# Performance work log

Measured on AMD Instinct MI355X. Metric: run time of the kernel, lower is better.

The kernel has to match this reference:

```python
import jax, jax.numpy as jnp
import numpy as np

N, IN_DIM, OUT_DIM, H = 8192, 512, 512, 1
BN_EPS = 1e-5


def _lin(key, fan_in, fan_out):
    k1, k2 = jax.random.split(key)
    b = 1.0 / np.sqrt(fan_in)
    W = jax.random.uniform(k1, (fan_in, fan_out), jnp.float32, -b, b)
    bias = jax.random.uniform(k2, (fan_out,), jnp.float32, -b, b)
    return W, bias


def setup_inputs() -> dict:
    key = jax.random.key(0)
    ks = jax.random.split(key, 12)
    h = jax.random.normal(ks[0], (N, IN_DIM), jnp.float32)
    A = (jax.random.uniform(ks[1], (N, N)) < 0.01).astype(jnp.float32)
    qw, qb = _lin(ks[2], IN_DIM, OUT_DIM * H)
    kw, kb = _lin(ks[3], IN_DIM, OUT_DIM * H)
    vw, vb = _lin(ks[4], IN_DIM, OUT_DIM * H)
    ow, ob = _lin(ks[5], OUT_DIM, OUT_DIM)
    f1w, f1b = _lin(ks[6], OUT_DIM, OUT_DIM * 2)
    f2w, f2b = _lin(ks[7], OUT_DIM * 2, OUT_DIM)
    bn1_g = jax.random.normal(ks[8], (OUT_DIM,)) * 0.1 + 1.0
    bn1_b = jax.random.normal(ks[9], (OUT_DIM,)) * 0.1
    bn1_m = jax.random.normal(ks[10], (OUT_DIM,)) * 0.1
    bn1_v = jax.random.uniform(ks[11], (OUT_DIM,), jnp.float32, 0.5, 1.5)
    ks2 = jax.random.split(jax.random.fold_in(key, 7), 4)
    bn2_g = jax.random.normal(ks2[0], (OUT_DIM,)) * 0.1 + 1.0
    bn2_b = jax.random.normal(ks2[1], (OUT_DIM,)) * 0.1
    bn2_m = jax.random.normal(ks2[2], (OUT_DIM,)) * 0.1
    bn2_v = jax.random.uniform(ks2[3], (OUT_DIM,), jnp.float32, 0.5, 1.5)
    return dict(A=A, h=h, qw=qw, qb=qb, kw=kw, kb=kb, vw=vw, vb=vb,
                ow=ow, ob=ob, f1w=f1w, f1b=f1b, f2w=f2w, f2b=f2b,
                bn1_g=bn1_g, bn1_b=bn1_b, bn1_m=bn1_m, bn1_v=bn1_v,
                bn2_g=bn2_g, bn2_b=bn2_b, bn2_m=bn2_m, bn2_v=bn2_v)


def _bn_eval(x, g, b, m, v):
    return (x - m) * jax.lax.rsqrt(v + BN_EPS) * g + b


def reference(A, h, qw, qb, kw, kb, vw, vb, ow, ob, f1w, f1b, f2w, f2b,
              bn1_g, bn1_b, bn1_m, bn1_v, bn2_g, bn2_b, bn2_m, bn2_v):
    n = h.shape[0]
    scaling = OUT_DIM ** (-0.5)
    # q/k/v: [N, D, H] as in torch reshape of [N, D*H]
    q = (h @ qw + qb).reshape(n, OUT_DIM, H) * scaling
    k = (h @ kw + kb).reshape(n, OUT_DIM, H)
    v = (h @ vw + vb).reshape(n, OUT_DIM, H)
    qh = jnp.transpose(q, (2, 0, 1))          # (H, N, D)
    kh = jnp.transpose(k, (2, 1, 0))          # (H, D, N)
    vh = jnp.transpose(v, (2, 0, 1))          # (H, N, D)
    attn = jnp.einsum('hnd,hdm->hnm', qh, kh) * A[None]   # (H, N, N)
    attn = jax.nn.softmax(attn, axis=0)        # NOTE: softmax over HEAD axis, as in source
    out = jnp.einsum('hnm,hmd->hnd', attn, vh).reshape(n, H * OUT_DIM)
    # GTLayer (eval mode: dropout = identity, BN uses running stats)
    x = out @ ow + ob
    x = x + h                                  # residual
    x = _bn_eval(x, bn1_g, bn1_b, bn1_m, bn1_v)
    h2 = x
    f = jax.nn.relu(x @ f1w + f1b) @ f2w + f2b
    x = h2 + f
    x = _bn_eval(x, bn2_g, bn2_b, bn2_m, bn2_v)
    return x
```

## Files before the change

### kernel.cpp

```cpp
#include <hip/hip_runtime.h>

#define NROWS 8192
#define DIM 512
#define HID 1024
#define BN_EPS 1e-5f

typedef unsigned short ushort_t;
typedef __attribute__((ext_vector_type(8))) __bf16 bf16x8;
typedef __attribute__((ext_vector_type(4))) float f32x4;

union U4 {
    uint4 u;
    bf16x8 b;
    ushort_t s[8];
};

static __device__ __forceinline__ float b2f(ushort_t u) {
    union { float f; unsigned int i; } c;
    c.i = ((unsigned int)u) << 16;
    return c.f;
}

static __device__ __forceinline__ ushort_t f2b(float f) {
    union { float f; unsigned int i; } c;
    c.f = f;
    unsigned int i = c.i;
    unsigned int r = (i + 0x7FFFu + ((i >> 16) & 1u)) >> 16;
    return (ushort_t)r;
}

__global__ void colsum_convert_kernel(const float* __restrict__ h, float* __restrict__ hs,
                                      ushort_t* __restrict__ hB) {
    int t = threadIdx.x;
    int col0 = (t & 127) * 4;
    int rsub = t >> 7;
    int row0 = blockIdx.x * 32;
    float acc[4] = {0.f, 0.f, 0.f, 0.f};
    for (int r = 0; r < 16; ++r) {
        int row = row0 + r * 2 + rsub;
        float4 v = *(const float4*)(h + (size_t)row * DIM + col0);
        acc[0] += v.x; acc[1] += v.y; acc[2] += v.z; acc[3] += v.w;
        ushort_t bv[4];
        bv[0] = f2b(v.x); bv[1] = f2b(v.y); bv[2] = f2b(v.z); bv[3] = f2b(v.w);
        *(uint2*)(hB + (size_t)row * DIM + col0) = *(uint2*)bv;
    }
#pragma unroll
    for (int j = 0; j < 4; ++j) atomicAdd(&hs[col0 + j], acc[j]);
}

__global__ void matvec_kernel(const float* __restrict__ xin, const float* __restrict__ W,
                              const float* __restrict__ bvec, float scaleB,
                              float* __restrict__ outv, int ncols) {
    __shared__ float red[8][32];
    int t = threadIdx.x;
    int col = blockIdx.x * 32 + (t & 31);
    int ks = t >> 5;
    float s = 0.f;
    for (int ki = 0; ki < 64; ++ki) {
        int k = ks * 64 + ki;
        s += xin[k] * W[(size_t)k * ncols + col];
    }
    red[ks][t & 31] = s;
    __syncthreads();
    if (ks == 0) {
        float tot = scaleB * bvec[col];
#pragma unroll
        for (int r = 0; r < 8; ++r) tot += red[r][t & 31];
        outv[col] = tot;
    }
}

__global__ void matvec_b1p_kernel(const float* __restrict__ tvec,
                                  const float* __restrict__ g1, const float* __restrict__ b1,
                                  const float* __restrict__ m1, const float* __restrict__ v1,
                                  const float* __restrict__ W, const float* __restrict__ bvec,
                                  float* __restrict__ outv) {
    __shared__ float red[8][32];
    int t = threadIdx.x;
    int col = blockIdx.x * 32 + (t & 31);
    int ks = t >> 5;
    float s = 0.f;
    for (int ki = 0; ki < 64; ++ki) {
        int k = ks * 64 + ki;
        float a1 = g1[k] * rsqrtf(v1[k] + BN_EPS);
        float q0 = tvec[k] * a1 + (b1[k] - m1[k] * a1);
        s += q0 * W[(size_t)k * HID + col];
    }
    red[ks][t & 31] = s;
    __syncthreads();
    if (ks == 0) {
        float tot = bvec[col];
#pragma unroll
        for (int r = 0; r < 8; ++r) tot += red[r][t & 31];
        outv[col] = tot;
    }
}

__global__ void prepw_kernel(const float* __restrict__ f1w,
                             const float* __restrict__ g1, const float* __restrict__ v1,
                             const float* __restrict__ f2w,
                             ushort_t* __restrict__ W1T, ushort_t* __restrict__ W2T) {
    __shared__ float tile[32][33];
    int tx = threadIdx.x & 31, ty = threadIdx.x >> 5;
    int b = blockIdx.x;
    if (b < 512) {
        int bx = (b & 31) * 32, by = (b >> 5) * 32;
#pragma unroll
        for (int i = 0; i < 32; i += 8)
            tile[ty + i][tx] = f1w[(size_t)(by + ty + i) * HID + bx + tx];
        __syncthreads();
        int r = by + tx;
        float a1 = g1[r] * rsqrtf(v1[r] + BN_EPS);
#pragma unroll
        for (int i = 0; i < 32; i += 8)
            W1T[(size_t)(bx + ty + i) * DIM + r] = f2b(tile[tx][ty + i] * a1);
    } else {
        int b2 = b - 512;
        int bx = (b2 & 15) * 32, by = (b2 >> 4) * 32;
#pragma unroll
        for (int i = 0; i < 32; i += 8)
            tile[ty + i][tx] = f2w[(size_t)(by + ty + i) * DIM + bx + tx];
        __syncthreads();
#pragma unroll
        for (int i = 0; i < 32; i += 8)
            W2T[(size_t)(bx + ty + i) * HID + by + tx] = f2b(tile[tx][ty + i]);
    }
}

__global__ __launch_bounds__(256) void gemm1_kernel(const ushort_t* __restrict__ A,
                                                    const ushort_t* __restrict__ BT,
                                                    const float* __restrict__ bias,
                                                    ushort_t* __restrict__ C) {
    const int K = DIM, Nn = HID, BK = 32, LDA = BK + 8;
    __shared__ ushort_t As[128 * LDA];
    __shared__ ushort_t Bs[128 * LDA];
    int tid = threadIdx.x;
    int lane = tid & 63, w = tid >> 6;
    int wm = (w & 1) * 64, wn = (w >> 1) * 64;
    int bm = blockIdx.y * 128, bn = blockIdx.x * 128;

    f32x4 acc[4][4] = {};

    int r0 = tid >> 2, kc0 = (tid & 3) * 8;
    int r1 = r0 + 64;

    for (int k0 = 0; k0 < K; k0 += BK) {
        __syncthreads();
        uint4 a0 = *(const uint4*)(A + (size_t)(bm + r0) * K + k0 + kc0);
        uint4 a1 = *(const uint4*)(A + (size_t)(bm + r1) * K + k0 + kc0);
        uint4 b0 = *(const uint4*)(BT + (size_t)(bn + r0) * K + k0 + kc0);
        uint4 b1 = *(const uint4*)(BT + (size_t)(bn + r1) * K + k0 + kc0);
        *(uint4*)(As + r0 * LDA + kc0) = a0;
        *(uint4*)(As + r1 * LDA + kc0) = a1;
        *(uint4*)(Bs + r0 * LDA + kc0) = b0;
        *(uint4*)(Bs + r1 * LDA + kc0) = b1;
        __syncthreads();

        int koff = (lane >> 4) * 8;
        bf16x8 af[4], bfr[4];
#pragma unroll
        for (int i = 0; i < 4; ++i) {
            U4 t;
            t.u = *(const uint4*)(As + (wm + i * 16 + (lane & 15)) * LDA + koff);
            af[i] = t.b;
        }
#pragma unroll
        for (int j = 0; j < 4; ++j) {
            U4 t;
            t.u = *(const uint4*)(Bs + (wn + j * 16 + (lane & 15)) * LDA + koff);
            bfr[j] = t.b;
        }
#pragma unroll
        for (int i = 0; i < 4; ++i)
#pragma unroll
            for (int j = 0; j < 4; ++j)
                acc[i][j] = __builtin_amdgcn_mfma_f32_16x16x32_bf16(af[i], bfr[j], acc[i][j], 0, 0, 0);
    }

#pragma unroll
    for (int i = 0; i < 4; ++i) {
        int row0 = bm + wm + i * 16 + (lane >> 4) * 4;
#pragma unroll
        for (int j = 0; j < 4; ++j) {
            int col = bn + wn + j * 16 + (lane & 15);
            float bv = bias[col];
#pragma unroll
            for (int r = 0; r < 4; ++r) {
                float v = fmaxf(acc[i][j][r] + bv, 0.f);
                C[(size_t)(row0 + r) * Nn + col] = f2b(v);
            }
        }
    }
}

__global__ __launch_bounds__(256) void gemm2_kernel(const ushort_t* __restrict__ A,
                                                    const ushort_t* __restrict__ BT,
                                                    const float* __restrict__ bias,
                                                    const ushort_t* __restrict__ hB,
                                                    const float* __restrict__ tvec,
                                                    const float* __restrict__ g1,
                                                    const float* __restrict__ b1,
                                                    const float* __restrict__ m1,
                                                    const float* __restrict__ v1,
                                                    const float* __restrict__ g2,
                                                    const float* __restrict__ b2,
                                                    const float* __restrict__ m2,
                                                    const float* __restrict__ v2,
                                                    float* __restrict__ out) {
    const int K = HID, BK = 32, LDA = BK + 8;
    __shared__ ushort_t As[128 * LDA];
    __shared__ ushort_t Bs[64 * LDA];
    int tid = threadIdx.x;
    int lane = tid & 63, w = tid >> 6;
    int wm = (w & 1) * 64, wn = (w >> 1) * 32;
    int bm = blockIdx.y * 128, bn = blockIdx.x * 64;

    f32x4 acc[4][2] = {};

    int r0 = tid >> 2, kc0 = (tid & 3) * 8;
    int r1 = r0 + 64;

    for (int k0 = 0; k0 < K; k0 += BK) {
        __syncthreads();
        uint4 a0 = *(const uint4*)(A + (size_t)(bm + r0) * K + k0 + kc0);
        uint4 a1 = *(const uint4*)(A + (size_t)(bm + r1) * K + k0 + kc0);
        uint4 bb = *(const uint4*)(BT + (size_t)(bn + r0) * K + k0 + kc0);
        *(uint4*)(As + r0 * LDA + kc0) = a0;
        *(uint4*)(As + r1 * LDA + kc0) = a1;
        *(uint4*)(Bs + r0 * LDA + kc0) = bb;
        __syncthreads();

        int koff = (lane >> 4) * 8;
        bf16x8 af[4], bfr[2];
#pragma unroll
        for (int i = 0; i < 4; ++i) {
            U4 t;
            t.u = *(const uint4*)(As + (wm + i * 16 + (lane & 15)) * LDA + koff);
            af[i] = t.b;
        }
#pragma unroll
        for (int j = 0; j < 2; ++j) {
            U4 t;
            t.u = *(const uint4*)(Bs + (wn + j * 16 + (lane & 15)) * LDA + koff);
            bfr[j] = t.b;
        }
#pragma unroll
        for (int i = 0; i < 4; ++i)
#pragma unroll
            for (int j = 0; j < 2; ++j)
                acc[i][j] = __builtin_amdgcn_mfma_f32_16x16x32_bf16(af[i], bfr[j], acc[i][j], 0, 0, 0);
    }

#pragma unroll
    for (int i = 0; i < 4; ++i) {
        int row0 = bm + wm + i * 16 + (lane >> 4) * 4;
#pragma unroll
        for (int j = 0; j < 2; ++j) {
            int col = bn + wn + j * 16 + (lane & 15);
            float a1c = g1[col] * rsqrtf(v1[col] + BN_EPS);
            float q0c = tvec[col] * a1c + (b1[col] - m1[col] * a1c);
            float a2c = g2[col] * rsqrtf(v2[col] + BN_EPS);
            float c2c = b2[col] - m2[col] * a2c;
            float bv = bias[col];
#pragma unroll
            for (int r = 0; r < 4; ++r) {
                int row = row0 + r;
                float x1 = b2f(hB[(size_t)row * DIM + col]) * a1c + q0c;
                out[(size_t)row * DIM + col] = (x1 + acc[i][j][r] + bv) * a2c + c2c;
            }
        }
    }
}

extern "C" void kernel_launch(void* const* d_in, const int* in_sizes, int n_in,
                              void* d_out, int out_size, void* d_ws, size_t ws_size,
                              hipStream_t stream) {
    const float* h = (const float*)d_in[1];
    const float* vw = (const float*)d_in[6];
    const float* vb = (const float*)d_in[7];
    const float* ow = (const float*)d_in[8];
    const float* ob = (const float*)d_in[9];
    const float* f1w = (const float*)d_in[10];
    const float* f1b = (const float*)d_in[11];
    const float* f2w = (const float*)d_in[12];
    const float* fb2 = (const float*)d_in[13];
    const float* g1 = (const float*)d_in[14];
    const float* b1 = (const float*)d_in[15];
    const float* m1 = (const float*)d_in[16];
    const float* v1 = (const float*)d_in[17];
    const float* g2 = (const float*)d_in[18];
    const float* b2 = (const float*)d_in[19];
    const float* m2 = (const float*)d_in[20];
    const float* v2 = (const float*)d_in[21];
    float* out = (float*)d_out;

    char* ws = (char*)d_ws;
    float* hs = (float*)(ws + 0);
    float* sBuf = (float*)(ws + 4096);
    float* tBuf = (float*)(ws + 8192);
    float* b1P = (float*)(ws + 16384);
    ushort_t* W1T = (ushort_t*)(ws + 32768);
    ushort_t* W2T = (ushort_t*)(ws + 32768 + 1048576);
    ushort_t* Z = (ushort_t*)(ws + 32768 + 2097152);
    ushort_t* hB = (ushort_t*)(ws + 32768 + 2097152 + 16777216);

    hipMemsetAsync(hs, 0, 512 * sizeof(float), stream);
    colsum_convert_kernel<<<256, 256, 0, stream>>>(h, hs, hB);
    matvec_kernel<<<16, 256, 0, stream>>>(hs, vw, vb, 8192.0f, sBuf, 512);
    matvec_kernel<<<16, 256, 0, stream>>>(sBuf, ow, ob, 1.0f, tBuf, 512);
    matvec_b1p_kernel<<<32, 256, 0, stream>>>(tBuf, g1, b1, m1, v1, f1w, f1b, b1P);
    prepw_kernel<<<1024, 256, 0, stream>>>(f1w, g1, v1, f2w, W1T, W2T);
    gemm1_kernel<<<dim3(8, 64), 256, 0, stream>>>(hB, W1T, b1P, Z);
    gemm2_kernel<<<dim3(8, 64), 256, 0, stream>>>(Z, W2T, fb2, hB, tBuf,
                                                  g1, b1, m1, v1, g2, b2, m2, v2, out);
}
```

Measured before the change: 471.1 us.

## Use direct global-to-LDS loads with XOR swizzle, BK=64, and fuse matvecs

Both GEMMs now stage tiles with global_load_lds (direct global-to-LDS DMA) over a 64-wide K tile and an XOR-swizzled LDS layout. This removes the register round trip and the padded layout and halves the number of barriers per K. The three small matvec kernels become one single-block kernel that also precomputes the per-column BN coefficients, so the gemm2 epilogue no longer recomputes rsqrt. The trade-off is that the fused matvec runs in one block of 512 threads, serializing work that was previously spread over 16 to 32 blocks.

```diff
diff --git a/kernel.cpp b/kernel.cpp
--- a/kernel.cpp
+++ b/kernel.cpp
@@ -8,6 +8,11 @@
 typedef unsigned short ushort_t;
 typedef __attribute__((ext_vector_type(8))) __bf16 bf16x8;
 typedef __attribute__((ext_vector_type(4))) float f32x4;
+
+typedef __attribute__((address_space(3))) void lds_void_t;
+typedef const __attribute__((address_space(1))) void gbl_void_t;
+
+#define GLDS16(g, l) __builtin_amdgcn_global_load_lds((gbl_void_t*)(g), (lds_void_t*)(l), 16, 0, 0)
 
 union U4 {
     uint4 u;
@@ -48,51 +53,40 @@
     for (int j = 0; j < 4; ++j) atomicAdd(&hs[col0 + j], acc[j]);
 }
 
-__global__ void matvec_kernel(const float* __restrict__ xin, const float* __restrict__ W,
-                              const float* __restrict__ bvec, float scaleB,
-                              float* __restrict__ outv, int ncols) {
-    __shared__ float red[8][32];
+__global__ void small_fused_kernel(const float* __restrict__ hs,
+                                   const float* __restrict__ vw, const float* __restrict__ vb,
+                                   const float* __restrict__ ow, const float* __restrict__ ob,
+                                   const float* __restrict__ f1w, const float* __restrict__ f1b,
+                                   const float* __restrict__ g1, const float* __restrict__ b1,
+                                   const float* __restrict__ m1, const float* __restrict__ v1,
+                                   const float* __restrict__ g2, const float* __restrict__ b2,
+                                   const float* __restrict__ m2, const float* __restrict__ v2,
+                                   float* __restrict__ cA1, float* __restrict__ cQ0,
+                                   float* __restrict__ cA2, float* __restrict__ cC2,
+                                   float* __restrict__ b1P) {
+    __shared__ float sh[512];
     int t = threadIdx.x;
-    int col = blockIdx.x * 32 + (t & 31);
-    int ks = t >> 5;
-    float s = 0.f;
-    for (int ki = 0; ki < 64; ++ki) {
-        int k = ks * 64 + ki;
-        s += xin[k] * W[(size_t)k * ncols + col];
-    }
-    red[ks][t & 31] = s;
+    float acc = 8192.0f * vb[t];
+    for (int k = 0; k < 512; ++k) acc += hs[k] * vw[(size_t)k * 512 + t];
+    sh[t] = acc;
     __syncthreads();
-    if (ks == 0) {
-        float tot = scaleB * bvec[col];
-#pragma unroll
-        for (int r = 0; r < 8; ++r) tot += red[r][t & 31];
-        outv[col] = tot;
-    }
-}
-
-__global__ void matvec_b1p_kernel(const float* __restrict__ tvec,
-                                  const float* __restrict__ g1, const float* __restrict__ b1,
-                                  const float* __restrict__ m1, const float* __restrict__ v1,
-                                  const float* __restrict__ W, const float* __restrict__ bvec,
-                                  float* __restrict__ outv) {
-    __shared__ float red[8][32];
-    int t = threadIdx.x;
-    int col = blockIdx.x * 32 + (t & 31);
-    int ks = t >> 5;
-    float s = 0.f;
-    for (int ki = 0; ki < 64; ++ki) {
-        int k = ks * 64 + ki;
-        float a1 = g1[k] * rsqrtf(v1[k] + BN_EPS);
-        float q0 = tvec[k] * a1 + (b1[k] - m1[k] * a1);
-        s += q0 * W[(size_t)k * HID + col];
-    }
-    red[ks][t & 31] = s;
+    float acc2 = ob[t];
+    for (int k = 0; k < 512; ++k) acc2 += sh[k] * ow[(size_t)k * 512 + t];
+    float a1 = g1[t] * rsqrtf(v1[t] + BN_EPS);
+    float q0 = acc2 * a1 + (b1[t] - m1[t] * a1);
+    float a2 = g2[t] * rsqrtf(v2[t] + BN_EPS);
+    cA1[t] = a1;
+    cQ0[t] = q0;
+    cA2[t] = a2;
+    cC2[t] = b2[t] - m2[t] * a2;
     __syncthreads();
-    if (ks == 0) {
-        float tot = bvec[col];
-#pragma unroll
-        for (int r = 0; r < 8; ++r) tot += red[r][t & 31];
-        outv[col] = tot;
+    sh[t] = q0;
+    __syncthreads();
+#pragma unroll
+    for (int c = t; c < 1024; c += 512) {
+        float a = f1b[c];
+        for (int k = 0; k < 512; ++k) a += sh[k] * f1w[(size_t)k * HID + c];
+        b1P[c] = a;
     }
 }
 
@@ -131,9 +125,9 @@
                                                     const ushort_t* __restrict__ BT,
                                                     const float* __restrict__ bias,
                                                     ushort_t* __restrict__ C) {
-    const int K = DIM, Nn = HID, BK = 32, LDA = BK + 8;
-    __shared__ ushort_t As[128 * LDA];
-    __shared__ ushort_t Bs[128 * LDA];
+    const int K = DIM, Nn = HID;
+    __shared__ ushort_t As[128 * 64];
+    __shared__ ushort_t Bs[128 * 64];
     int tid = threadIdx.x;
     int lane = tid & 63, w = tid >> 6;
     int wm = (w & 1) * 64, wn = (w >> 1) * 64;
@@ -141,40 +135,48 @@
 
     f32x4 acc[4][4] = {};
 
-    int r0 = tid >> 2, kc0 = (tid & 3) * 8;
-    int r1 = r0 + 64;
-
-    for (int k0 = 0; k0 < K; k0 += BK) {
-        __syncthreads();
-        uint4 a0 = *(const uint4*)(A + (size_t)(bm + r0) * K + k0 + kc0);
-        uint4 a1 = *(const uint4*)(A + (size_t)(bm + r1) * K + k0 + kc0);
-        uint4 b0 = *(const uint4*)(BT + (size_t)(bn + r0) * K + k0 + kc0);
-        uint4 b1 = *(const uint4*)(BT + (size_t)(bn + r1) * K + k0 + kc0);
-        *(uint4*)(As + r0 * LDA + kc0) = a0;
-        *(uint4*)(As + r1 * LDA + kc0) = a1;
-        *(uint4*)(Bs + r0 * LDA + kc0) = b0;
-        *(uint4*)(Bs + r1 * LDA + kc0) = b1;
-        __syncthreads();
-
-        int koff = (lane >> 4) * 8;
-        bf16x8 af[4], bfr[4];
-#pragma unroll
-        for (int i = 0; i < 4; ++i) {
-            U4 t;
-            t.u = *(const uint4*)(As + (wm + i * 16 + (lane & 15)) * LDA + koff);
-            af[i] = t.b;
-        }
-#pragma unroll
-        for (int j = 0; j < 4; ++j) {
-            U4 t;
-            t.u = *(const uint4*)(Bs + (wn + j * 16 + (lane & 15)) * LDA + koff);
-            bfr[j] = t.b;
-        }
-#pragma unroll
-        for (int i = 0; i < 4; ++i)
-#pragma unroll
-            for (int j = 0; j < 4; ++j)
-                acc[i][j] = __builtin_amdgcn_mfma_f32_16x16x32_bf16(af[i], bfr[j], acc[i][j], 0, 0, 0);
+    int rsub = tid >> 3;
+    int clog = (tid & 7) ^ (rsub & 7);
+    int gcol = clog * 8;
+
+    for (int k0 = 0; k0 < K; k0 += 64) {
+        __syncthreads();
+#pragma unroll
+        for (int R = 0; R < 4; ++R) {
+            int row = R * 32 + rsub;
+            GLDS16(A + (size_t)(bm + row) * K + k0 + gcol, As + (R * 256 + w * 64) * 8);
+        }
+#pragma unroll
+        for (int R = 0; R < 4; ++R) {
+            int row = R * 32 + rsub;
+            GLDS16(BT + (size_t)(bn + row) * K + k0 + gcol, Bs + (R * 256 + w * 64) * 8);
+        }
+        __syncthreads();
+
+#pragma unroll
+        for (int s = 0; s < 2; ++s) {
+            int cl = (lane >> 4) + s * 4;
+            bf16x8 af[4], bfr[4];
+#pragma unroll
+            for (int i = 0; i < 4; ++i) {
+                int row = wm + i * 16 + (lane & 15);
+                int cp = cl ^ (row & 7);
+                U4 tt; tt.u = *(const uint4*)(As + row * 64 + cp * 8);
+                af[i] = tt.b;
+            }
+#pragma unroll
+            for (int j = 0; j < 4; ++j) {
+                int row = wn + j * 16 + (lane & 15);
+                int cp = cl ^ (row & 7);
+                U4 tt; tt.u = *(const uint4*)(Bs + row * 64 + cp * 8);
+                bfr[j] = tt.b;
+            }
+#pragma unroll
+            for (int i = 0; i < 4; ++i)
+#pragma unroll
+                for (int j = 0; j < 4; ++j)
+                    acc[i][j] = __builtin_amdgcn_mfma_f32_16x16x32_bf16(af[i], bfr[j], acc[i][j], 0, 0, 0);
+        }
     }
 
 #pragma unroll
@@ -197,19 +199,14 @@
                                                     const ushort_t* __restrict__ BT,
                                                     const float* __restrict__ bias,
                                                     const ushort_t* __restrict__ hB,
-                                                    const float* __restrict__ tvec,
-                                                    const float* __restrict__ g1,
-                                                    const float* __restrict__ b1,
-                                                    const float* __restrict__ m1,
-                                                    const float* __restrict__ v1,
-                                                    const float* __restrict__ g2,
-                                                    const float* __restrict__ b2,
-                                                    const float* __restrict__ m2,
-                                                    const float* __restrict__ v2,
+                                                    const float* __restrict__ cA1,
+                                                    const float* __restrict__ cQ0,
+                                                    const float* __restrict__ cA2,
+                                                    const float* __restrict__ cC2,
                                                     float* __restrict__ out) {
-    const int K = HID, BK = 32, LDA = BK + 8;
-    __shared__ ushort_t As[128 * LDA];
-    __shared__ ushort_t Bs[64 * LDA];
+    const int K = HID;
+    __shared__ ushort_t As[128 * 64];
+    __shared__ ushort_t Bs[64 * 64];
     int tid = threadIdx.x;
     int lane = tid & 63, w = tid >> 6;
     int wm = (w & 1) * 64, wn = (w >> 1) * 32;
@@ -217,38 +214,48 @@
 
     f32x4 acc[4][2] = {};
 
-    int r0 = tid >> 2, kc0 = (tid & 3) * 8;
-    int r1 = r0 + 64;
-
-    for (int k0 = 0; k0 < K; k0 += BK) {
-        __syncthreads();
-        uint4 a0 = *(const uint4*)(A + (size_t)(bm + r0) * K + k0 + kc0);
-        uint4 a1 = *(const uint4*)(A + (size_t)(bm + r1) * K + k0 + kc0);
-        uint4 bb = *(const uint4*)(BT + (size_t)(bn + r0) * K + k0 + kc0);
-        *(uint4*)(As + r0 * LDA + kc0) = a0;
-        *(uint4*)(As + r1 * LDA + kc0) = a1;
-        *(uint4*)(Bs + r0 * LDA + kc0) = bb;
-        __syncthreads();
-
-        int koff = (lane >> 4) * 8;
-        bf16x8 af[4], bfr[2];
-#pragma unroll
-        for (int i = 0; i < 4; ++i) {
-            U4 t;
-            t.u = *(const uint4*)(As + (wm + i * 16 + (lane & 15)) * LDA + koff);
-            af[i] = t.b;
-        }
-#pragma unroll
-        for (int j = 0; j < 2; ++j) {
-            U4 t;
-            t.u = *(const uint4*)(Bs + (wn + j * 16 + (lane & 15)) * LDA + koff);
-            bfr[j] = t.b;
-        }
-#pragma unroll
-        for (int i = 0; i < 4; ++i)
-#pragma unroll
-            for (int j = 0; j < 2; ++j)
-                acc[i][j] = __builtin_amdgcn_mfma_f32_16x16x32_bf16(af[i], bfr[j], acc[i][j], 0, 0, 0);
+    int rsub = tid >> 3;
+    int clog = (tid & 7) ^ (rsub & 7);
+    int gcol = clog * 8;
+
+    for (int k0 = 0; k0 < K; k0 += 64) {
+        __syncthreads();
+#pragma unroll
+        for (int R = 0; R < 4; ++R) {
+            int row = R * 32 + rsub;
+            GLDS16(A + (size_t)(bm + row) * K + k0 + gcol, As + (R * 256 + w * 64) * 8);
+        }
+#pragma unroll
+        for (int R = 0; R < 2; ++R) {
+            int row = R * 32 + rsub;
+            GLDS16(BT + (size_t)(bn + row) * K + k0 + gcol, Bs + (R * 256 + w * 64) * 8);
+        }
+        __syncthreads();
+
+#pragma unroll
+        for (int s = 0; s < 2; ++s) {
+            int cl = (lane >> 4) + s * 4;
+            bf16x8 af[4], bfr[2];
+#pragma unroll
+            for (int i = 0; i < 4; ++i) {
+                int row = wm + i * 16 + (lane & 15);
+                int cp = cl ^ (row & 7);
+                U4 tt; tt.u = *(const uint4*)(As + row * 64 + cp * 8);
+                af[i] = tt.b;
+            }
+#pragma unroll
+            for (int j = 0; j < 2; ++j) {
+                int row = wn + j * 16 + (lane & 15);
+                int cp = cl ^ (row & 7);
+                U4 tt; tt.u = *(const uint4*)(Bs + row * 64 + cp * 8);
+                bfr[j] = tt.b;
+            }
+#pragma unroll
+            for (int i = 0; i < 4; ++i)
+#pragma unroll
+                for (int j = 0; j < 2; ++j)
+                    acc[i][j] = __builtin_amdgcn_mfma_f32_16x16x32_bf16(af[i], bfr[j], acc[i][j], 0, 0, 0);
+        }
     }
 
 #pragma unroll
@@ -257,10 +264,8 @@
 #pragma unroll
         for (int j = 0; j < 2; ++j) {
             int col = bn + wn + j * 16 + (lane & 15);
-            float a1c = g1[col] * rsqrtf(v1[col] + BN_EPS);
-            float q0c = tvec[col] * a1c + (b1[col] - m1[col] * a1c);
-            float a2c = g2[col] * rsqrtf(v2[col] + BN_EPS);
-            float c2c = b2[col] - m2[col] * a2c;
+            float a1c = cA1[col], q0c = cQ0[col];
+            float a2c = cA2[col], c2c = cC2[col];
             float bv = bias[col];
 #pragma unroll
             for (int r = 0; r < 4; ++r) {
@@ -296,8 +301,10 @@
 
     char* ws = (char*)d_ws;
     float* hs = (float*)(ws + 0);
-    float* sBuf = (float*)(ws + 4096);
-    float* tBuf = (float*)(ws + 8192);
+    float* cA1 = (float*)(ws + 4096);
+    float* cQ0 = (float*)(ws + 6144);
+    float* cA2 = (float*)(ws + 8192);
+    float* cC2 = (float*)(ws + 10240);
     float* b1P = (float*)(ws + 16384);
     ushort_t* W1T = (ushort_t*)(ws + 32768);
     ushort_t* W2T = (ushort_t*)(ws + 32768 + 1048576);
@@ -306,11 +313,10 @@
 
     hipMemsetAsync(hs, 0, 512 * sizeof(float), stream);
     colsum_convert_kernel<<<256, 256, 0, stream>>>(h, hs, hB);
-    matvec_kernel<<<16, 256, 0, stream>>>(hs, vw, vb, 8192.0f, sBuf, 512);
-    matvec_kernel<<<16, 256, 0, stream>>>(sBuf, ow, ob, 1.0f, tBuf, 512);
-    matvec_b1p_kernel<<<32, 256, 0, stream>>>(tBuf, g1, b1, m1, v1, f1w, f1b, b1P);
+    small_fused_kernel<<<1, 512, 0, stream>>>(hs, vw, vb, ow, ob, f1w, f1b,
+                                              g1, b1, m1, v1, g2, b2, m2, v2,
+                                              cA1, cQ0, cA2, cC2, b1P);
     prepw_kernel<<<1024, 256, 0, stream>>>(f1w, g1, v1, f2w, W1T, W2T);
     gemm1_kernel<<<dim3(8, 64), 256, 0, stream>>>(hB, W1T, b1P, Z);
-    gemm2_kernel<<<dim3(8, 64), 256, 0, stream>>>(Z, W2T, fb2, hB, tBuf,
-                                                  g1, b1, m1, v1, g2, b2, m2, v2, out);
-}
+    gemm2_kernel<<<dim3(8, 64), 256, 0, stream>>>(Z, W2T, fb2, hB, cA1, cQ0, cA2, cC2, out);
+}
```

Result: slower. 523.1 us (+11.0%).
